# Optimization experiments

Measured on AMD Instinct MI355X. Metric: run time of the kernel, lower is better.

The kernel has to match this reference:

```python
import jax, jax.numpy as jnp
import numpy as np

U = 200000      # unique nodes
B = 20000       # node_list batch size
K = 33          # n_nbr_samples + self
F = 256         # feature_dim
E = 128         # emb_dim
BN_EPS = 1e-5


def setup_inputs() -> dict:
    key = jax.random.key(0)
    k1, k2, k3, k4 = jax.random.split(key, 4)
    return {
        "features": jax.random.normal(k1, (U, F), dtype=jnp.float32),
        "W": jax.random.normal(k2, (F, E), dtype=jnp.float32) * 0.05,
        "b": jax.random.normal(k3, (E,), dtype=jnp.float32) * 0.01,
        "gamma": jnp.ones((E,), dtype=jnp.float32),
        "beta": jnp.zeros((E,), dtype=jnp.float32),
        "sample_idx": jax.random.randint(k4, (B, K), 0, U, dtype=jnp.int64)
        if jax.config.jax_enable_x64 else jax.random.randint(k4, (B, K), 0, U, dtype=jnp.int32),
    }


def reference(features, W, b, gamma, beta, sample_idx):
    # fc: Linear -> BatchNorm1d (training-mode batch stats) -> Tanh; Dropout in eval (identity)
    h = features @ W + b                       # [U, E]
    mu = jnp.mean(h, axis=0)                   # [E]
    var = jnp.var(h, axis=0)                   # biased var, as torch BN uses for normalization
    h = jnp.tanh(gamma * (h - mu) * jax.lax.rsqrt(var + BN_EPS) + beta)  # [U, E]
    # Row-normalized 0/1 mask matmul == mean over the K distinct sampled unique-node rows
    gathered = h[sample_idx]                   # [B, K, E] irregular gather
    return jnp.mean(gathered, axis=1)          # [B, E]
```

## Files before the change

kernel.cpp:

```cpp
#include <hip/hip_runtime.h>

#define U_NODES 200000
#define B_ROWS  20000
#define K_S     33
#define F_DIM   256
#define E_DIM   128
#define NBLK    1563

typedef __bf16 bf16x8 __attribute__((ext_vector_type(8)));
typedef float  f32x4  __attribute__((ext_vector_type(4)));
typedef unsigned short ushortx4 __attribute__((ext_vector_type(4)));
typedef unsigned short ushortx8 __attribute__((ext_vector_type(8)));

__device__ __forceinline__ unsigned short f2bf(float f) {
    unsigned int u = __builtin_bit_cast(unsigned int, f);
    u += 0x7fffu + ((u >> 16) & 1u);
    return (unsigned short)(u >> 16);
}
__device__ __forceinline__ float bf2f(unsigned short s) {
    return __builtin_bit_cast(float, ((unsigned int)s) << 16);
}
__device__ __forceinline__ bf16x8 pack_bf8(f32x4 a, f32x4 b) {
    ushortx8 r;
    r[0] = f2bf(a[0]); r[1] = f2bf(a[1]); r[2] = f2bf(a[2]); r[3] = f2bf(a[3]);
    r[4] = f2bf(b[0]); r[5] = f2bf(b[1]); r[6] = f2bf(b[2]); r[7] = f2bf(b[3]);
    return __builtin_bit_cast(bf16x8, r);
}

__global__ void wprep_kernel(const float* __restrict__ W, unsigned short* __restrict__ Wt) {
    int n = blockIdx.x;
    int k = threadIdx.x;
    Wt[n * F_DIM + k] = f2bf(W[(size_t)k * E_DIM + n]);
}

__global__ __launch_bounds__(256) void gemm_stats_kernel(
    const float* __restrict__ A, const unsigned short* __restrict__ Wt,
    unsigned short* __restrict__ h, float* __restrict__ partial)
{
    __shared__ __attribute__((aligned(16))) char smem[65536];
    char* Ws = smem;

    const int t    = threadIdx.x;
    const int lane = t & 63;
    const int wv   = t >> 6;
    const int m    = lane & 15;
    const int qd   = lane >> 4;
    const int row0 = blockIdx.x * 128;

    int gr0 = row0 + wv * 32 + m;       if (gr0 >= U_NODES) gr0 = U_NODES - 1;
    int gr1 = row0 + wv * 32 + 16 + m;  if (gr1 >= U_NODES) gr1 = U_NODES - 1;
    const float* pa0 = A + (size_t)gr0 * F_DIM + qd * 8;
    const float* pa1 = A + (size_t)gr1 * F_DIM + qd * 8;

#define LOAD_CHUNK(P, c) do {                                                  \
        P[0] = *(const f32x4*)(pa0 + (c) * 64);                                \
        P[1] = *(const f32x4*)(pa0 + (c) * 64 + 4);                            \
        P[2] = *(const f32x4*)(pa0 + (c) * 64 + 32);                           \
        P[3] = *(const f32x4*)(pa0 + (c) * 64 + 36);                           \
        P[4] = *(const f32x4*)(pa1 + (c) * 64);                                \
        P[5] = *(const f32x4*)(pa1 + (c) * 64 + 4);                            \
        P[6] = *(const f32x4*)(pa1 + (c) * 64 + 32);                           \
        P[7] = *(const f32x4*)(pa1 + (c) * 64 + 36);                           \
    } while (0)

#define COMPUTE_CHUNK(P, c) do {                                               \
        bf16x8 a00 = pack_bf8(P[0], P[1]);                                     \
        bf16x8 a01 = pack_bf8(P[2], P[3]);                                     \
        bf16x8 a10 = pack_bf8(P[4], P[5]);                                     \
        bf16x8 a11 = pack_bf8(P[6], P[7]);                                     \
        _Pragma("unroll")                                                      \
        for (int ct = 0; ct < 8; ++ct) {                                       \
            int rb = ct * 16 + m;                                              \
            bf16x8 b0 = *(const bf16x8*)(Ws + rb * 512 +                       \
                            ((((c) * 8 + qd) ^ (rb & 7)) << 4));               \
            acc0[ct] = __builtin_amdgcn_mfma_f32_16x16x32_bf16(a00, b0, acc0[ct], 0, 0, 0); \
            acc1[ct] = __builtin_amdgcn_mfma_f32_16x16x32_bf16(a10, b0, acc1[ct], 0, 0, 0); \
            bf16x8 b1 = *(const bf16x8*)(Ws + rb * 512 +                       \
                            ((((c) * 8 + 4 + qd) ^ (rb & 7)) << 4));           \
            acc0[ct] = __builtin_amdgcn_mfma_f32_16x16x32_bf16(a01, b1, acc0[ct], 0, 0, 0); \
            acc1[ct] = __builtin_amdgcn_mfma_f32_16x16x32_bf16(a11, b1, acc1[ct], 0, 0, 0); \
        }                                                                      \
    } while (0)

    f32x4 p0[8], p1[8];
    LOAD_CHUNK(p0, 0);

    #pragma unroll
    for (int i = 0; i < 16; ++i) {
        int flat = t + 256 * i;
        int r = flat >> 5, q = flat & 31;
        ushortx8 v = *(const ushortx8*)(Wt + (size_t)r * F_DIM + q * 8);
        *(ushortx8*)(Ws + r * 512 + ((q ^ (r & 7)) << 4)) = v;
    }

    f32x4 acc0[8], acc1[8];
    #pragma unroll
    for (int ct = 0; ct < 8; ++ct) {
        acc0[ct] = (f32x4){0.f, 0.f, 0.f, 0.f};
        acc1[ct] = (f32x4){0.f, 0.f, 0.f, 0.f};
    }

    __syncthreads();

    LOAD_CHUNK(p1, 1);
    COMPUTE_CHUNK(p0, 0);
    LOAD_CHUNK(p0, 2);
    COMPUTE_CHUNK(p1, 1);
    LOAD_CHUNK(p1, 3);
    COMPUTE_CHUNK(p0, 2);
    COMPUTE_CHUNK(p1, 3);

#undef LOAD_CHUNK
#undef COMPUTE_CHUNK

    __syncthreads();

    const bool full = (row0 + 128) <= U_NODES;
    float s[8], sq[8];
    #pragma unroll
    for (int ct = 0; ct < 8; ++ct) {
        float ss = 0.f, qq = 0.f;
        #pragma unroll
        for (int v = 0; v < 4; ++v) {
            float x0 = acc0[ct][v];
            float x1 = acc1[ct][v];
            if (full || (row0 + wv * 32 + qd * 4 + v) < U_NODES)      { ss += x0; qq += x0 * x0; }
            if (full || (row0 + wv * 32 + 16 + qd * 4 + v) < U_NODES) { ss += x1; qq += x1 * x1; }
        }
        s[ct] = ss; sq[ct] = qq;
    }
    float* redS = (float*)smem;
    float* redQ = (float*)(smem + 8192);
    int rq = wv * 4 + qd;
    #pragma unroll
    for (int ct = 0; ct < 8; ++ct) {
        redS[rq * 128 + ct * 16 + m] = s[ct];
        redQ[rq * 128 + ct * 16 + m] = sq[ct];
    }
    __syncthreads();
    {
        float tot = 0.f;
        if (t < 128) {
            #pragma unroll
            for (int i = 0; i < 16; ++i) tot += redS[i * 128 + t];
        } else {
            #pragma unroll
            for (int i = 0; i < 16; ++i) tot += redQ[i * 128 + (t - 128)];
        }
        partial[(size_t)blockIdx.x * 256 + t] = tot;
    }
    __syncthreads();

    unsigned short* tb = (unsigned short*)(smem + wv * 8192);
    #pragma unroll
    for (int ct = 0; ct < 8; ++ct)
        #pragma unroll
        for (int v = 0; v < 4; ++v) {
            tb[(qd * 4 + v) * 128 + ct * 16 + m]        = f2bf(acc0[ct][v]);
            tb[(16 + qd * 4 + v) * 128 + ct * 16 + m]   = f2bf(acc1[ct][v]);
        }
    __syncthreads();
    #pragma unroll
    for (int i = 0; i < 8; ++i) {
        int idx = lane + 64 * i;
        int r = idx >> 4, c8 = (idx & 15) * 8;
        int gr = row0 + wv * 32 + r;
        if (gr < U_NODES)
            *(ushortx8*)(h + (size_t)gr * E_DIM + c8) = *(const ushortx8*)(tb + r * 128 + c8);
    }
}

__global__ __launch_bounds__(256) void reduce_kernel(
    const float* __restrict__ partial, float* __restrict__ gsum, float* __restrict__ gsq)
{
    __shared__ float red[256];
    const int c = blockIdx.x;
    const int t = threadIdx.x;
    float acc = 0.f;
    for (int j = t; j < NBLK; j += 256) acc += partial[(size_t)j * 256 + c];
    red[t] = acc;
    __syncthreads();
    #pragma unroll
    for (int s = 128; s > 0; s >>= 1) {
        if (t < s) red[t] += red[t + s];
        __syncthreads();
    }
    if (t == 0) {
        if (c < 128) gsum[c] = red[0];
        else         gsq[c - 128] = red[0];
    }
}

__global__ void finalize_kernel(const float* __restrict__ gsum, const float* __restrict__ gsq,
                                const float* __restrict__ gamma, const float* __restrict__ beta,
                                float* __restrict__ scale, float* __restrict__ shift)
{
    int e = threadIdx.x;
    float mu  = gsum[e] * (1.f / U_NODES);
    float var = gsq[e] * (1.f / U_NODES) - mu * mu;
    float inv = rsqrtf(var + 1e-5f);
    float sc  = gamma[e] * inv;
    scale[e] = sc;
    shift[e] = beta[e] - sc * mu;
}

__global__ __launch_bounds__(256) void gather_kernel(
    const unsigned short* __restrict__ h, const int* __restrict__ sidx_g,
    const float* __restrict__ scale, const float* __restrict__ shift,
    float* __restrict__ out)
{
    __shared__ int sl[16 * K_S];
    const int t  = threadIdx.x;
    const int g  = t & 15;
    const int r  = t >> 4;
    const int b0 = blockIdx.x * 16;
    for (int i = t; i < 16 * K_S; i += 256) sl[i] = sidx_g[(size_t)b0 * K_S + i];
    float scv[8], shv[8];
    *(float4*)&scv[0] = *(const float4*)(scale + g * 8);
    *(float4*)&scv[4] = *(const float4*)(scale + g * 8 + 4);
    *(float4*)&shv[0] = *(const float4*)(shift + g * 8);
    *(float4*)&shv[4] = *(const float4*)(shift + g * 8 + 4);
    __syncthreads();

    float acc[8] = {0.f, 0.f, 0.f, 0.f, 0.f, 0.f, 0.f, 0.f};
    #pragma unroll
    for (int k = 0; k < K_S; ++k) {
        int idx = sl[r * K_S + k];
        ushortx8 v = *(const ushortx8*)(h + (size_t)idx * E_DIM + g * 8);
        #pragma unroll
        for (int j = 0; j < 8; ++j) {
            float x  = bf2f(v[j]) * scv[j] + shv[j];
            float ex = __expf(2.f * x);
            acc[j] += 1.f - 2.f * __builtin_amdgcn_rcpf(ex + 1.f);
        }
    }
    float* op = out + (size_t)(b0 + r) * E_DIM + g * 8;
    *(float4*)(op)     = make_float4(acc[0] * (1.f / K_S), acc[1] * (1.f / K_S),
                                     acc[2] * (1.f / K_S), acc[3] * (1.f / K_S));
    *(float4*)(op + 4) = make_float4(acc[4] * (1.f / K_S), acc[5] * (1.f / K_S),
                                     acc[6] * (1.f / K_S), acc[7] * (1.f / K_S));
}

extern "C" void kernel_launch(void* const* d_in, const int* in_sizes, int n_in,
                              void* d_out, int out_size, void* d_ws, size_t ws_size,
                              hipStream_t stream) {
    const float* features = (const float*)d_in[0];
    const float* W        = (const float*)d_in[1];
    const float* gamma    = (const float*)d_in[3];
    const float* beta     = (const float*)d_in[4];
    const int*   sample   = (const int*)d_in[5];
    float* out = (float*)d_out;

    float* gsum    = (float*)d_ws;
    float* gsq     = gsum + 128;
    float* scale   = gsq + 128;
    float* shift   = scale + 128;
    float* partial = shift + 128;
    unsigned short* Wt = (unsigned short*)(partial + (size_t)NBLK * 256);
    unsigned short* h  = Wt + 128 * 256;

    wprep_kernel<<<128, 256, 0, stream>>>(W, Wt);
    gemm_stats_kernel<<<NBLK, 256, 0, stream>>>(features, Wt, h, partial);
    reduce_kernel<<<256, 256, 0, stream>>>(partial, gsum, gsq);
    finalize_kernel<<<1, 128, 0, stream>>>(gsum, gsq, gamma, beta, scale, shift);
    gather_kernel<<<B_ROWS / 16, 256, 0, stream>>>(h, sample, scale, shift, out);
}
```

Measured before the change: 341.5 us.

## Issue all feature chunk loads upfront and fuse reduce with finalize kernel

The GEMM kernel now issues all four feature-chunk loads before the weight staging and barrier instead of double-buffering, so more memory requests are in flight at once. The cost is more live registers, which may lower occupancy. The separate stats reduce and finalize kernels are merged into one 128-block kernel that sums and squares per column and writes scale/shift directly, saving a launch and the intermediate buffers.

```diff
diff --git a/kernel.cpp b/kernel.cpp
--- a/kernel.cpp
+++ b/kernel.cpp
@@ -82,8 +82,11 @@
         }                                                                      \
     } while (0)
 
-    f32x4 p0[8], p1[8];
-    LOAD_CHUNK(p0, 0);
+    f32x4 pA[8], pB[8], pC[8], pD[8];
+    LOAD_CHUNK(pA, 0);
+    LOAD_CHUNK(pB, 1);
+    LOAD_CHUNK(pC, 2);
+    LOAD_CHUNK(pD, 3);
 
     #pragma unroll
     for (int i = 0; i < 16; ++i) {
@@ -102,13 +105,10 @@
 
     __syncthreads();
 
-    LOAD_CHUNK(p1, 1);
-    COMPUTE_CHUNK(p0, 0);
-    LOAD_CHUNK(p0, 2);
-    COMPUTE_CHUNK(p1, 1);
-    LOAD_CHUNK(p1, 3);
-    COMPUTE_CHUNK(p0, 2);
-    COMPUTE_CHUNK(p1, 3);
+    COMPUTE_CHUNK(pA, 0);
+    COMPUTE_CHUNK(pB, 1);
+    COMPUTE_CHUNK(pC, 2);
+    COMPUTE_CHUNK(pD, 3);
 
 #undef LOAD_CHUNK
 #undef COMPUTE_CHUNK
@@ -170,38 +170,34 @@
     }
 }
 
-__global__ __launch_bounds__(256) void reduce_kernel(
-    const float* __restrict__ partial, float* __restrict__ gsum, float* __restrict__ gsq)
+__global__ __launch_bounds__(256) void reduce_finalize_kernel(
+    const float* __restrict__ partial,
+    const float* __restrict__ gamma, const float* __restrict__ beta,
+    float* __restrict__ scale, float* __restrict__ shift)
 {
-    __shared__ float red[256];
+    __shared__ float redS[256], redQ[256];
     const int c = blockIdx.x;
     const int t = threadIdx.x;
-    float acc = 0.f;
-    for (int j = t; j < NBLK; j += 256) acc += partial[(size_t)j * 256 + c];
-    red[t] = acc;
+    float a = 0.f, b = 0.f;
+    for (int j = t; j < NBLK; j += 256) {
+        a += partial[(size_t)j * 256 + c];
+        b += partial[(size_t)j * 256 + c + 128];
+    }
+    redS[t] = a; redQ[t] = b;
     __syncthreads();
     #pragma unroll
     for (int s = 128; s > 0; s >>= 1) {
-        if (t < s) red[t] += red[t + s];
+        if (t < s) { redS[t] += redS[t + s]; redQ[t] += redQ[t + s]; }
         __syncthreads();
     }
     if (t == 0) {
-        if (c < 128) gsum[c] = red[0];
-        else         gsq[c - 128] = red[0];
-    }
-}
-
-__global__ void finalize_kernel(const float* __restrict__ gsum, const float* __restrict__ gsq,
-                                const float* __restrict__ gamma, const float* __restrict__ beta,
-                                float* __restrict__ scale, float* __restrict__ shift)
-{
-    int e = threadIdx.x;
-    float mu  = gsum[e] * (1.f / U_NODES);
-    float var = gsq[e] * (1.f / U_NODES) - mu * mu;
-    float inv = rsqrtf(var + 1e-5f);
-    float sc  = gamma[e] * inv;
-    scale[e] = sc;
-    shift[e] = beta[e] - sc * mu;
+        float mu  = redS[0] * (1.f / U_NODES);
+        float var = redQ[0] * (1.f / U_NODES) - mu * mu;
+        float inv = rsqrtf(var + 1e-5f);
+        float sc  = gamma[c] * inv;
+        scale[c] = sc;
+        shift[c] = beta[c] - sc * mu;
+    }
 }
 
 __global__ __launch_bounds__(256) void gather_kernel(
@@ -251,9 +247,7 @@
     const int*   sample   = (const int*)d_in[5];
     float* out = (float*)d_out;
 
-    float* gsum    = (float*)d_ws;
-    float* gsq     = gsum + 128;
-    float* scale   = gsq + 128;
+    float* scale   = (float*)d_ws;
     float* shift   = scale + 128;
     float* partial = shift + 128;
     unsigned short* Wt = (unsigned short*)(partial + (size_t)NBLK * 256);
@@ -261,7 +255,6 @@
 
     wprep_kernel<<<128, 256, 0, stream>>>(W, Wt);
     gemm_stats_kernel<<<NBLK, 256, 0, stream>>>(features, Wt, h, partial);
-    reduce_kernel<<<256, 256, 0, stream>>>(partial, gsum, gsq);
-    finalize_kernel<<<1, 128, 0, stream>>>(gsum, gsq, gamma, beta, scale, shift);
+    reduce_finalize_kernel<<<128, 256, 0, stream>>>(partial, gamma, beta, scale, shift);
     gather_kernel<<<B_ROWS / 16, 256, 0, stream>>>(h, sample, scale, shift, out);
 }
```

Result: slower. 360.9 us (+5.7%).
